# Optimization experiments

Hardware: AMD Instinct MI355X
Metric: run time of the kernel (lower is better)

## Reference

```python
import jax, jax.numpy as jnp
import numpy as np

EPS = 1e-5


def _conv1x1(h, w, b):
    # 1x1 conv == per-pixel matmul: (b,c,h,w) x (o,c) -> (b,o,h,w)
    return jnp.einsum('bchw,oc->bohw', h, w) + b[None, :, None, None]


def setup_inputs() -> dict:
    key = jax.random.key(0)
    ks = jax.random.split(key, 7)
    B, C, H, W = 4, 512, 64, 64
    s = 0.02
    return {
        'x': jax.random.normal(ks[0], (B, C, H, W), dtype=jnp.float32),
        'wq': jax.random.normal(ks[1], (C, C), dtype=jnp.float32) * s,
        'bq': jax.random.normal(ks[2], (C,), dtype=jnp.float32) * s,
        'wk': jax.random.normal(ks[3], (C, C), dtype=jnp.float32) * s,
        'bk': jax.random.normal(ks[4], (C,), dtype=jnp.float32) * s,
        'wv': jax.random.normal(ks[5], (C, C), dtype=jnp.float32) * s,
        'bv': jax.random.normal(ks[6], (C,), dtype=jnp.float32) * s,
    }


def reference(x, wq, bq, wk, bk, wv, bv):
    B, C, H, W = x.shape
    # InstanceNorm2d (affine=False): normalize over spatial dims per (b, c)
    mu = jnp.mean(x, axis=(2, 3), keepdims=True)
    var = jnp.var(x, axis=(2, 3), keepdims=True)  # biased, matches torch
    h_ = (x - mu) * jax.lax.rsqrt(var + EPS)

    q = _conv1x1(h_, wq, bq).reshape(B, C, H * W)  # (b, c, n)
    k = _conv1x1(h_, wk, bk).reshape(B, C, H * W)
    v = _conv1x1(h_, wv, bv).reshape(B, C, H * W)

    scale = float(int(C)) ** (-0.5)
    attn = jnp.einsum('bcq,bck->bqk', q, k) * scale  # (b, n_q, n_k)
    attn = jax.nn.softmax(attn, axis=-1)
    # torch: bmm(v, attn.permute(0,2,1)) -> A[b,c,q] = sum_k v[b,c,k] * attn[b,q,k]
    A = jnp.einsum('bck,bqk->bcq', v, attn).reshape(B, C, H, W)
    return x + A
```

## Files before the change

### kernel.cpp

```cpp
#include <hip/hip_runtime.h>
#include <hip/hip_bf16.h>
#include <cstdint>

#define B_ 4
#define C_ 512
#define N_ 4096

typedef unsigned short u16;
typedef __bf16 bf16x8 __attribute__((ext_vector_type(8)));
typedef float f32x4 __attribute__((ext_vector_type(4)));

union U16B { uint4 u; bf16x8 v; };

__device__ __forceinline__ bf16x8 ld16g(const u16* p) {
  U16B t; t.u = *(const uint4*)p; return t.v;
}

__device__ __forceinline__ u16 f2bf(float f) {
  uint32_t u = __builtin_bit_cast(uint32_t, f);
  u = (u + 0x7FFFu + ((u >> 16) & 1u)) >> 16;
  return (u16)u;
}
__device__ __forceinline__ float bf2f(u16 h) {
  uint32_t u = ((uint32_t)h) << 16;
  return __builtin_bit_cast(float, u);
}

typedef const __attribute__((address_space(1))) uint32_t* gas_p;
typedef __attribute__((address_space(3))) uint32_t* las_p;
__device__ __forceinline__ void gld16(const void* g, void* l) {
  __builtin_amdgcn_global_load_lds((gas_p)g, (las_p)l, 16, 0, 0);
}

#define SCEXP 0.06376149809794171f

__global__ __launch_bounds__(256) void cvt_w(const float* __restrict__ w, u16* __restrict__ o) {
  int i = blockIdx.x * 256 + threadIdx.x;
  float4 v = ((const float4*)w)[i];
  ushort4 r;
  r.x = f2bf(v.x); r.y = f2bf(v.y); r.z = f2bf(v.z); r.w = f2bf(v.w);
  ((ushort4*)o)[i] = r;
}

__global__ __launch_bounds__(1024) void pack_bias(const float* __restrict__ bq,
    const float* __restrict__ bk, float* __restrict__ o) {
  int i = threadIdx.x;
  o[i] = (i < 512) ? bq[i] : bk[i - 512];
}

__global__ __launch_bounds__(256) void inorm_stats(const float* __restrict__ x,
    float* __restrict__ mu, float* __restrict__ rstd) {
  int bc = blockIdx.x;
  const float4* p = (const float4*)(x + (size_t)bc * N_);
  float s = 0.f, ss = 0.f;
  for (int i = threadIdx.x; i < N_ / 4; i += 256) {
    float4 v = p[i];
    s  += v.x + v.y + v.z + v.w;
    ss += v.x * v.x + v.y * v.y + v.z * v.z + v.w * v.w;
  }
#pragma unroll
  for (int off = 32; off > 0; off >>= 1) {
    s  += __shfl_down(s, off);
    ss += __shfl_down(ss, off);
  }
  __shared__ float as_[4], ass_[4];
  if ((threadIdx.x & 63) == 0) { as_[threadIdx.x >> 6] = s; ass_[threadIdx.x >> 6] = ss; }
  __syncthreads();
  if (threadIdx.x == 0) {
    float S  = as_[0] + as_[1] + as_[2] + as_[3];
    float SS = ass_[0] + ass_[1] + ass_[2] + ass_[3];
    float m  = S * (1.f / N_);
    float var = SS * (1.f / N_) - m * m;
    mu[bc] = m;
    rstd[bc] = rsqrtf(var + 1e-5f);
  }
}

__global__ __launch_bounds__(256) void norm_transpose(const float* __restrict__ x,
    const float* __restrict__ mu, const float* __restrict__ rstd, u16* __restrict__ hT) {
  __shared__ u16 tile[64][66];
  int b = blockIdx.z, c0 = blockIdx.y * 64, n0 = blockIdx.x * 64;
  int tn = threadIdx.x & 63, t4 = threadIdx.x >> 6;
  const float* xb = x + ((size_t)b * C_ + c0) * N_ + n0;
#pragma unroll
  for (int it = 0; it < 16; ++it) {
    int c = t4 + it * 4;
    float m  = mu[b * C_ + c0 + c];
    float rs = rstd[b * C_ + c0 + c];
    tile[c][tn] = f2bf((xb[(size_t)c * N_ + tn] - m) * rs);
  }
  __syncthreads();
  u16* hTb = hT + ((size_t)b * N_ + n0) * C_ + c0;
#pragma unroll
  for (int it = 0; it < 16; ++it) {
    int n = t4 + it * 4;
    hTb[(size_t)n * C_ + tn] = tile[tn][n];
  }
}

#define EPI_BCOL 0
#define EPI_BROW 1

template<int EPI>
__global__ __launch_bounds__(256) void gemm128(
    const u16* __restrict__ A, const u16* __restrict__ B,
    const float* __restrict__ aux, void* __restrict__ Out,
    int klen, int lda, int ldb, int ldo,
    long sAz, long sBz, long sOz)
{
  int z = blockIdx.z;
  const u16* Ab = A + (size_t)z * sAz;
  const u16* Bb = B + (size_t)z * sBz;
  int m0 = blockIdx.x * 128, n0 = blockIdx.y * 128;
  int t = threadIdx.x, w = t >> 6, l = t & 63;
  int wr = w >> 1, wc = w & 1;
  int l16 = l & 15, lg = l >> 4;

  __shared__ char smem[65536];

  int srow = t >> 3;
  int scol = ((t & 7) << 4) ^ ((srow & 7) << 4);
  size_t ldaB = (size_t)lda * 2, ldbB = (size_t)ldb * 2;

  f32x4 acc[4][4] = {};
  int nsteps = klen >> 6;

#define STAGE(step, d) {                                                     \
    size_t kbyte = (size_t)(step) * 128 + scol;                              \
    char* lb = smem + (d) * 32768;                                           \
    _Pragma("unroll")                                                        \
    for (int i = 0; i < 4; ++i) {                                            \
      int row = i * 32 + srow;                                               \
      gld16((const char*)Ab + (size_t)(m0 + row) * ldaB + kbyte,             \
            lb + (size_t)(i * 256 + t) * 16);                                \
      gld16((const char*)Bb + (size_t)(n0 + row) * ldbB + kbyte,             \
            lb + 16384 + (size_t)(i * 256 + t) * 16);                        \
    }                                                                        \
  }

  STAGE(0, 0);
  __syncthreads();
  int cur = 0;
  int sw = (l16 & 7) << 4;
  for (int s = 0; s < nsteps; ++s) {
    if (s + 1 < nsteps) STAGE(s + 1, cur ^ 1);
    const char* Al = smem + cur * 32768;
    const char* Bl = Al + 16384;
#pragma unroll
    for (int kc = 0; kc < 2; ++kc) {
      int cb = (kc * 64 + lg * 16) ^ sw;
      bf16x8 af[4], bf[4];
#pragma unroll
      for (int mf = 0; mf < 4; ++mf)
        af[mf] = *(const bf16x8*)(Al + (wr * 64 + mf * 16 + l16) * 128 + cb);
#pragma unroll
      for (int nf = 0; nf < 4; ++nf)
        bf[nf] = *(const bf16x8*)(Bl + (wc * 64 + nf * 16 + l16) * 128 + cb);
#pragma unroll
      for (int mf = 0; mf < 4; ++mf)
#pragma unroll
        for (int nf = 0; nf < 4; ++nf)
          acc[mf][nf] = __builtin_amdgcn_mfma_f32_16x16x32_bf16(af[mf], bf[nf], acc[mf][nf], 0, 0, 0);
    }
    __syncthreads();
    cur ^= 1;
  }
#undef STAGE

  u16* ob = (u16*)Out + (size_t)z * sOz;
  float bc[4];
  if constexpr (EPI == EPI_BCOL) {
#pragma unroll
    for (int nf = 0; nf < 4; ++nf) bc[nf] = aux[n0 + wc * 64 + nf * 16 + l16];
  }
#pragma unroll
  for (int mf = 0; mf < 4; ++mf) {
#pragma unroll
    for (int nf = 0; nf < 4; ++nf) {
      int col = n0 + wc * 64 + nf * 16 + l16;
#pragma unroll
      for (int r = 0; r < 4; ++r) {
        int row = m0 + wr * 64 + mf * 16 + lg * 4 + r;
        float v = acc[mf][nf][r] + (EPI == EPI_BCOL ? bc[nf] : aux[row]);
        ob[(size_t)row * ldo + col] = f2bf(v);
      }
    }
  }
}


#define STG32(Ab, Bb, ldab, step, lb) {                                      \
    size_t kb = (size_t)(step) * 64;                                         \
    _Pragma("unroll")                                                        \
    for (int i = 0; i < 2; ++i) {                                            \
      int s2 = i * 256 + t;                                                  \
      int row = s2 >> 2;                                                     \
      int sc = (((s2 & 3) ^ ((row >> 1) & 3)) & 3) << 4;                     \
      gld16((const char*)(Ab) + (size_t)(m0 + row) * (ldab) + kb + sc,       \
            (lb) + (size_t)s2 * 16);                                         \
      gld16((const char*)(Bb) + (size_t)(n0 + row) * (ldab) + kb + sc,       \
            (lb) + 8192 + (size_t)s2 * 16);                                  \
    }                                                                        \
  }

#define COMP32(lb) {                                                         \
    const char* Al = (lb);                                                   \
    const char* Bl = (lb) + 8192;                                            \
    bf16x8 af[4], bf[4];                                                     \
    _Pragma("unroll")                                                        \
    for (int mf = 0; mf < 4; ++mf)                                           \
      af[mf] = *(const bf16x8*)(Al + (wr * 64 + mf * 16 + l16) * 64 + rg);   \
    _Pragma("unroll")                                                        \
    for (int nf = 0; nf < 4; ++nf)                                           \
      bf[nf] = *(const bf16x8*)(Bl + (wc * 64 + nf * 16 + l16) * 64 + rg);   \
    _Pragma("unroll")                                                        \
    for (int mf = 0; mf < 4; ++mf)                                           \
      _Pragma("unroll")                                                      \
      for (int nf = 0; nf < 4; ++nf)                                         \
        acc[mf][nf] = __builtin_amdgcn_mfma_f32_16x16x32_bf16(af[mf], bf[nf], acc[mf][nf], 0, 0, 0); \
  }

__global__ __launch_bounds__(256, 3) void exp128(
    const u16* __restrict__ qk, float* __restrict__ dsumAll, u16* __restrict__ Pall)
{
  int fid = blockIdx.x;
  int rid = (fid & 7) * 512 + (fid >> 3);
  int z = rid >> 10;
  int r10 = rid & 1023;
  int st = r10 >> 6, w6 = r10 & 63;
  int m0 = ((st >> 2) * 8 + (w6 >> 3)) * 128;
  int n0 = ((st & 3) * 8 + (w6 & 7)) * 128;

  const u16* Ab = qk + (size_t)z * ((size_t)N_ * 1024);
  const u16* Bb = Ab + 512;
  float* dsum = dsumAll + (size_t)z * N_;
  u16* Pp = Pall + (size_t)z * (size_t)N_ * N_;

  int t = threadIdx.x, w = t >> 6, l = t & 63;
  int wr = w >> 1, wc = w & 1;
  int l16 = l & 15, lg = l >> 4;

  __shared__ char smem[49152];

  f32x4 acc[4][4] = {};
  int rg = ((lg ^ ((l16 >> 1) & 3)) & 3) << 4;

  char* buf0 = smem;
  char* buf1 = smem + 16384;
  char* buf2 = smem + 32768;

  STG32(Ab, Bb, 2048, 0, buf0);
  STG32(Ab, Bb, 2048, 1, buf1);
#pragma unroll
  for (int s = 0; s < 15; ++s) {
    asm volatile("s_waitcnt vmcnt(4)" ::: "memory");
    __builtin_amdgcn_s_barrier();
    __builtin_amdgcn_sched_barrier(0);
    if (s + 2 < 16) STG32(Ab, Bb, 2048, s + 2, buf2);
    COMP32(buf0);
    char* tmp = buf0; buf0 = buf1; buf1 = buf2; buf2 = tmp;
  }
  asm volatile("s_waitcnt vmcnt(0)" ::: "memory");
  __builtin_amdgcn_s_barrier();
  __builtin_amdgcn_sched_barrier(0);
  COMP32(buf0);

  __syncthreads();
#pragma unroll
  for (int mf = 0; mf < 4; ++mf) {
#pragma unroll
    for (int r = 0; r < 4; ++r) {
      int row = wr * 64 + mf * 16 + lg * 4 + r;
      int swz = ((row >> 2) & 3) << 5;
      float rs = 0.f;
#pragma unroll
      for (int nf = 0; nf < 4; ++nf) {
        int colb = wc * 128 + nf * 32 + l16 * 2;
        float p = __builtin_amdgcn_exp2f(acc[mf][nf][r] * SCEXP);
        u16 pb = f2bf(p);
        *(u16*)(smem + row * 256 + (colb ^ swz)) = pb;
        rs += bf2f(pb);
      }
      rs += __shfl_xor(rs, 1); rs += __shfl_xor(rs, 2);
      rs += __shfl_xor(rs, 4); rs += __shfl_xor(rs, 8);
      if (l16 == 0) atomicAdd(&dsum[m0 + row], rs);
    }
  }
  __syncthreads();
#pragma unroll
  for (int it = 0; it < 8; ++it) {
    int idx = it * 256 + t;
    int row = idx >> 4, g = idx & 15;
    uint4 v = *(const uint4*)(smem + row * 256 + ((g * 16) ^ (((row >> 2) & 3) << 5)));
    *(uint4*)(Pp + ((size_t)(m0 + row) * N_ + n0 + g * 8)) = v;
  }
}

__global__ __launch_bounds__(256, 3) void pv128(
    const u16* __restrict__ vM, const u16* __restrict__ P,
    const float* __restrict__ denom, const float* __restrict__ x,
    float* __restrict__ out)
{
  int fid = blockIdx.x;
  int rid = (fid & 7) * 64 + (fid >> 3);
  int z = rid >> 7;
  int r7 = rid & 127;
  int n0 = (r7 >> 2) * 128;
  int m0 = (r7 & 3) * 128;

  const u16* Ab = vM + (size_t)z * ((size_t)C_ * N_);
  const u16* Bb = P + (size_t)z * ((size_t)N_ * N_);
  const float* db = denom + (size_t)z * N_;
  const float* xb = x + (size_t)z * ((size_t)C_ * N_);
  float* ob = out + (size_t)z * ((size_t)C_ * N_);

  int t = threadIdx.x, w = t >> 6, l = t & 63;
  int wr = w >> 1, wc = w & 1;
  int l16 = l & 15, lg = l >> 4;

  __shared__ char smem[49152];

  f32x4 acc[4][4] = {};
  int rg = ((lg ^ ((l16 >> 1) & 3)) & 3) << 4;

  char* buf0 = smem;
  char* buf1 = smem + 16384;
  char* buf2 = smem + 32768;

  STG32(Ab, Bb, 8192, 0, buf0);
  STG32(Ab, Bb, 8192, 1, buf1);
#pragma unroll 3
  for (int s = 0; s < 127; ++s) {
    asm volatile("s_waitcnt vmcnt(4)" ::: "memory");
    __builtin_amdgcn_s_barrier();
    __builtin_amdgcn_sched_barrier(0);
    if (s + 2 < 128) STG32(Ab, Bb, 8192, s + 2, buf2);
    COMP32(buf0);
    char* tmp = buf0; buf0 = buf1; buf1 = buf2; buf2 = tmp;
  }
  asm volatile("s_waitcnt vmcnt(0)" ::: "memory");
  __builtin_amdgcn_s_barrier();
  __builtin_amdgcn_sched_barrier(0);
  COMP32(buf0);

  float rd[4];
#pragma unroll
  for (int nf = 0; nf < 4; ++nf)
    rd[nf] = 1.0f / db[n0 + wc * 64 + nf * 16 + l16];
#pragma unroll
  for (int mf = 0; mf < 4; ++mf) {
#pragma unroll
    for (int r = 0; r < 4; ++r) {
      int row = m0 + wr * 64 + mf * 16 + lg * 4 + r;
#pragma unroll
      for (int nf = 0; nf < 4; ++nf) {
        int col = n0 + wc * 64 + nf * 16 + l16;
        size_t o = (size_t)row * N_ + col;
        ob[o] = xb[o] + acc[mf][nf][r] * rd[nf];
      }
    }
  }
}

__global__ __launch_bounds__(256) void gemm_abT(
    const u16* __restrict__ A, const u16* __restrict__ Bm,
    const float* __restrict__ bias, u16* __restrict__ out,
    int ldo, int bias_is_row)
{
  int w = threadIdx.x >> 6, l = threadIdx.x & 63;
  int l16 = l & 15, lg = l >> 4;
  int m0 = blockIdx.x * 128 + (w >> 1) * 64;
  int n0 = blockIdx.y * 128 + (w & 1) * 64;
  f32x4 acc[4][4] = {};
  const u16* Ab = A  + (size_t)(m0 + l16) * 512 + lg * 8;
  const u16* Bb = Bm + (size_t)(n0 + l16) * 512 + lg * 8;
  for (int kc = 0; kc < 512; kc += 32) {
    bf16x8 af[4], bf[4];
#pragma unroll
    for (int i = 0; i < 4; ++i) af[i] = ld16g(Ab + (size_t)(i * 16) * 512 + kc);
#pragma unroll
    for (int j = 0; j < 4; ++j) bf[j] = ld16g(Bb + (size_t)(j * 16) * 512 + kc);
#pragma unroll
    for (int i = 0; i < 4; ++i)
#pragma unroll
      for (int j = 0; j < 4; ++j)
        acc[i][j] = __builtin_amdgcn_mfma_f32_16x16x32_bf16(af[i], bf[j], acc[i][j], 0, 0, 0);
  }
#pragma unroll
  for (int i = 0; i < 4; ++i) {
#pragma unroll
    for (int j = 0; j < 4; ++j) {
      int col = n0 + j * 16 + l16;
#pragma unroll
      for (int r = 0; r < 4; ++r) {
        int row = m0 + i * 16 + lg * 4 + r;
        float v = acc[i][j][r] + (bias_is_row ? bias[row] : bias[col]);
        out[(size_t)row * ldo + col] = f2bf(v);
      }
    }
  }
}

#define NQ 32
#define NKB 64
__global__ __launch_bounds__(512) void attn_kernel(
    const u16* __restrict__ qT, const u16* __restrict__ kT, const u16* __restrict__ vM,
    const float* __restrict__ x, float* __restrict__ out)
{
  int b = blockIdx.y;
  int nq0 = blockIdx.x * NQ;
  const u16* qTb = qT + (size_t)b * N_ * C_;
  const u16* kTb = kT + (size_t)b * N_ * C_;
  const u16* vb  = vM + (size_t)b * C_ * N_;
  const float* xb = x + (size_t)b * C_ * N_;
  float* ob = out + (size_t)b * C_ * N_;

  int tid = threadIdx.x;
  int w = tid >> 6, l = tid & 63, l16 = l & 15, lg = l >> 4;
  int nqf = w & 1, nkf = w >> 1;
  int c0 = w * 64;

  __shared__ u16 qlds[32][520];
  __shared__ u16 Plds[32][72];
  __shared__ float dpart[32][16];
  __shared__ float dfin[32];

  for (int idx = tid; idx < 32 * 64; idx += 512) {
    int row = idx >> 6, cg = idx & 63;
    *(uint4*)&qlds[row][cg * 8] = *(const uint4*)(qTb + (size_t)(nq0 + row) * C_ + cg * 8);
  }
  __syncthreads();

  f32x4 acc[2][4] = {};
  float dreg = 0.f;
  int drow = tid >> 4, dcol = (tid & 15) * 4;

  for (int nk0 = 0; nk0 < N_; nk0 += NKB) {
    f32x4 s = {0.f, 0.f, 0.f, 0.f};
    const u16* krow = kTb + (size_t)(nk0 + nkf * 16 + l16) * C_ + lg * 8;
#pragma unroll 4
    for (int kc = 0; kc < 16; ++kc) {
      U16B tq; tq.u = *(const uint4*)&qlds[nqf * 16 + l16][kc * 32 + lg * 8];
      bf16x8 kf = ld16g(krow + kc * 32);
      s = __builtin_amdgcn_mfma_f32_16x16x32_bf16(tq.v, kf, s, 0, 0, 0);
    }
    __syncthreads();
#pragma unroll
    for (int r = 0; r < 4; ++r) {
      float p = __builtin_amdgcn_exp2f(s[r] * SCEXP);
      Plds[nqf * 16 + lg * 4 + r][nkf * 16 + l16] = f2bf(p);
    }
    __syncthreads();
#pragma unroll
    for (int r = 0; r < 4; ++r) dreg += bf2f(Plds[drow][dcol + r]);
#pragma unroll
    for (int kk = 0; kk < 2; ++kk) {
      bf16x8 pf[2];
#pragma unroll
      for (int i = 0; i < 2; ++i) {
        U16B t2; t2.u = *(const uint4*)&Plds[i * 16 + l16][kk * 32 + lg * 8];
        pf[i] = t2.v;
      }
#pragma unroll
      for (int j = 0; j < 4; ++j) {
        bf16x8 vf = ld16g(vb + (size_t)(c0 + j * 16 + l16) * N_ + nk0 + kk * 32 + lg * 8);
#pragma unroll
        for (int i = 0; i < 2; ++i)
          acc[i][j] = __builtin_amdgcn_mfma_f32_16x16x32_bf16(pf[i], vf, acc[i][j], 0, 0, 0);
      }
    }
  }

  dpart[drow][tid & 15] = dreg;
  __syncthreads();
  if (tid < 32) {
    float s2 = 0.f;
#pragma unroll
    for (int g = 0; g < 16; ++g) s2 += dpart[tid][g];
    dfin[tid] = s2;
  }
  __syncthreads();

#pragma unroll
  for (int i = 0; i < 2; ++i) {
    float dinv[4];
#pragma unroll
    for (int r = 0; r < 4; ++r) dinv[r] = 1.f / dfin[i * 16 + lg * 4 + r];
    int nbase = nq0 + i * 16 + lg * 4;
#pragma unroll
    for (int j = 0; j < 4; ++j) {
      int c = c0 + j * 16 + l16;
      float4 xv = *(const float4*)(xb + (size_t)c * N_ + nbase);
      float4 o;
      o.x = xv.x + acc[i][j][0] * dinv[0];
      o.y = xv.y + acc[i][j][1] * dinv[1];
      o.z = xv.z + acc[i][j][2] * dinv[2];
      o.w = xv.w + acc[i][j][3] * dinv[3];
      *(float4*)(ob + (size_t)c * N_ + nbase) = o;
    }
  }
}

extern "C" void kernel_launch(void* const* d_in, const int* in_sizes, int n_in,
                              void* d_out, int out_size, void* d_ws, size_t ws_size,
                              hipStream_t stream) {
  (void)in_sizes; (void)n_in; (void)out_size;
  const float* x  = (const float*)d_in[0];
  const float* wq = (const float*)d_in[1];
  const float* bq = (const float*)d_in[2];
  const float* wk = (const float*)d_in[3];
  const float* bk = (const float*)d_in[4];
  const float* wv = (const float*)d_in[5];
  const float* bv = (const float*)d_in[6];
  float* out = (float*)d_out;
  char* ws = (char*)d_ws;

  const size_t NC = (size_t)N_ * C_;
  const size_t NEED = 203489280;

  if (ws_size >= NEED) {
    u16*   wbf_q = (u16*)(ws);
    u16*   wbf_k = (u16*)(ws + 524288);
    u16*   wbf_v = (u16*)(ws + 1048576);
    float* bqk   = (float*)(ws + 1572864);
    float* mu    = (float*)(ws + 1581056);
    float* rstd  = (float*)(ws + 1589248);
    u16*   hT    = (u16*)(ws + 1597440);
    u16*   qkT   = (u16*)(ws + 18874368);
    u16*   vM    = (u16*)(ws + 52428800);
    float* denom = (float*)(ws + 69206016);
    u16*   P     = (u16*)(ws + 69271552);

    cvt_w<<<256, 256, 0, stream>>>(wq, wbf_q);
    cvt_w<<<256, 256, 0, stream>>>(wk, wbf_k);
    cvt_w<<<256, 256, 0, stream>>>(wv, wbf_v);
    pack_bias<<<1, 1024, 0, stream>>>(bq, bk, bqk);
    inorm_stats<<<B_ * C_, 256, 0, stream>>>(x, mu, rstd);
    norm_transpose<<<dim3(N_ / 64, C_ / 64, B_), 256, 0, stream>>>(x, mu, rstd, hT);
    hipMemsetAsync(denom, 0, 4 * N_ * sizeof(float), stream);

    gemm128<EPI_BCOL><<<dim3(32, 8, 4), 256, 0, stream>>>(
        hT, wbf_q, bqk, qkT, 512, 512, 512, 1024, (long)NC, 0, (long)N_ * 1024);
    gemm128<EPI_BROW><<<dim3(4, 32, 4), 256, 0, stream>>>(
        wbf_v, hT, bv, vM, 512, 512, 512, 4096, 0, (long)NC, (long)NC);

    exp128<<<4096, 256, 0, stream>>>(qkT, denom, P);

    pv128<<<512, 256, 0, stream>>>(vM, P, denom, x, out);
  } else {
    u16*   wbf_q = (u16*)(ws);
    u16*   wbf_k = (u16*)(ws + 524288);
    u16*   wbf_v = (u16*)(ws + 1048576);
    float* mu    = (float*)(ws + 1572864);
    float* rstd  = (float*)(ws + 1581056);
    u16*   hT    = (u16*)(ws + 1589248);
    u16*   qT    = (u16*)(ws + 18366464);
    u16*   kT    = (u16*)(ws + 35143680);
    u16*   vM    = (u16*)(ws + 51920896);

    cvt_w<<<256, 256, 0, stream>>>(wq, wbf_q);
    cvt_w<<<256, 256, 0, stream>>>(wk, wbf_k);
    cvt_w<<<256, 256, 0, stream>>>(wv, wbf_v);
    inorm_stats<<<B_ * C_, 256, 0, stream>>>(x, mu, rstd);
    norm_transpose<<<dim3(N_ / 64, C_ / 64, B_), 256, 0, stream>>>(x, mu, rstd, hT);

    for (int b = 0; b < B_; ++b) {
      const u16* hTb = hT + (size_t)b * NC;
      u16* qTb = qT + (size_t)b * NC;
      u16* kTb = kT + (size_t)b * NC;
      u16* vMb = vM + (size_t)b * NC;
      gemm_abT<<<dim3(N_ / 128, C_ / 128), 256, 0, stream>>>(hTb, wbf_q, bq, qTb, C_, 0);
      gemm_abT<<<dim3(N_ / 128, C_ / 128), 256, 0, stream>>>(hTb, wbf_k, bk, kTb, C_, 0);
      gemm_abT<<<dim3(C_ / 128, N_ / 128), 256, 0, stream>>>(wbf_v, hTb, bv, vMb, N_, 1);
    }
    attn_kernel<<<dim3(N_ / NQ, B_), 512, 0, stream>>>(qT, kT, vM, x, out);
  }
}
```

Measured before the change: 240.8 us.

## Widen QK^T exp kernel tile to 128x256 with four column-split waves

Replaces the 128x128 score/exp kernel with a 128x256 tile where each of four waves owns a 64-column strip and all 128 rows, doubling per-wave accumulators. This halves the number of blocks and the re-reading of the Q tile per output, improving arithmetic intensity of the K-loop. It costs more registers and LDS (72KB), lowers occupancy to 2 blocks/SM, and changes the block swizzle mapping.

```diff
diff --git a/kernel.cpp b/kernel.cpp
--- a/kernel.cpp
+++ b/kernel.cpp
@@ -220,16 +220,16 @@
         acc[mf][nf] = __builtin_amdgcn_mfma_f32_16x16x32_bf16(af[mf], bf[nf], acc[mf][nf], 0, 0, 0); \
   }
 
-__global__ __launch_bounds__(256, 3) void exp128(
+__global__ __launch_bounds__(256, 2) void exp_wide(
     const u16* __restrict__ qk, float* __restrict__ dsumAll, u16* __restrict__ Pall)
 {
   int fid = blockIdx.x;
-  int rid = (fid & 7) * 512 + (fid >> 3);
-  int z = rid >> 10;
-  int r10 = rid & 1023;
-  int st = r10 >> 6, w6 = r10 & 63;
-  int m0 = ((st >> 2) * 8 + (w6 >> 3)) * 128;
-  int n0 = ((st & 3) * 8 + (w6 & 7)) * 128;
+  int rid = (fid & 7) * 256 + (fid >> 3);
+  int z = rid >> 9;
+  int r9 = rid & 511;
+  int st = r9 >> 6, w6 = r9 & 63;
+  int m0 = ((st >> 1) * 8 + (w6 >> 3)) * 128;
+  int n0 = ((st & 1) * 8 + (w6 & 7)) * 256;
 
   const u16* Ab = qk + (size_t)z * ((size_t)N_ * 1024);
   const u16* Bb = Ab + 512;
@@ -237,40 +237,79 @@
   u16* Pp = Pall + (size_t)z * (size_t)N_ * N_;
 
   int t = threadIdx.x, w = t >> 6, l = t & 63;
-  int wr = w >> 1, wc = w & 1;
+  int wc = w;
   int l16 = l & 15, lg = l >> 4;
 
-  __shared__ char smem[49152];
-
-  f32x4 acc[4][4] = {};
+  __shared__ char smem[73728];
+
+  f32x4 acc[8][4] = {};
   int rg = ((lg ^ ((l16 >> 1) & 3)) & 3) << 4;
 
+#define STGW(step, lb) {                                                     \
+    size_t kb = (size_t)(step) * 64;                                         \
+    _Pragma("unroll")                                                        \
+    for (int i = 0; i < 2; ++i) {                                            \
+      int s2 = i * 256 + t;                                                  \
+      int row = s2 >> 2;                                                     \
+      int sc = (((s2 & 3) ^ ((row >> 1) & 3)) & 3) << 4;                     \
+      gld16((const char*)Ab + (size_t)(m0 + row) * 2048 + kb + sc,           \
+            (lb) + (size_t)s2 * 16);                                         \
+    }                                                                        \
+    _Pragma("unroll")                                                        \
+    for (int i = 0; i < 4; ++i) {                                            \
+      int s2 = i * 256 + t;                                                  \
+      int row = s2 >> 2;                                                     \
+      int sc = (((s2 & 3) ^ ((row >> 1) & 3)) & 3) << 4;                     \
+      gld16((const char*)Bb + (size_t)(n0 + row) * 2048 + kb + sc,           \
+            (lb) + 8192 + (size_t)s2 * 16);                                  \
+    }                                                                        \
+  }
+
+#define COMPW(lb) {                                                         \
+    const char* Al = (lb);                                                  \
+    const char* Bl = (lb) + 8192;                                           \
+    bf16x8 af[8], bf[4];                                                    \
+    _Pragma("unroll")                                                       \
+    for (int mf = 0; mf < 8; ++mf)                                          \
+      af[mf] = *(const bf16x8*)(Al + (mf * 16 + l16) * 64 + rg);            \
+    _Pragma("unroll")                                                       \
+    for (int nf = 0; nf < 4; ++nf)                                          \
+      bf[nf] = *(const bf16x8*)(Bl + (wc * 64 + nf * 16 + l16) * 64 + rg);  \
+    _Pragma("unroll")                                                       \
+    for (int mf = 0; mf < 8; ++mf)                                          \
+      _Pragma("unroll")                                                     \
+      for (int nf = 0; nf < 4; ++nf)                                        \
+        acc[mf][nf] = __builtin_amdgcn_mfma_f32_16x16x32_bf16(af[mf], bf[nf], acc[mf][nf], 0, 0, 0); \
+  }
+
   char* buf0 = smem;
-  char* buf1 = smem + 16384;
-  char* buf2 = smem + 32768;
-
-  STG32(Ab, Bb, 2048, 0, buf0);
-  STG32(Ab, Bb, 2048, 1, buf1);
-#pragma unroll
+  char* buf1 = smem + 24576;
+  char* buf2 = smem + 49152;
+
+  STGW(0, buf0);
+  STGW(1, buf1);
+#pragma unroll 3
   for (int s = 0; s < 15; ++s) {
-    asm volatile("s_waitcnt vmcnt(4)" ::: "memory");
+    asm volatile("s_waitcnt vmcnt(6)" ::: "memory");
     __builtin_amdgcn_s_barrier();
     __builtin_amdgcn_sched_barrier(0);
-    if (s + 2 < 16) STG32(Ab, Bb, 2048, s + 2, buf2);
-    COMP32(buf0);
+    if (s + 2 < 16) STGW(s + 2, buf2);
+    COMPW(buf0);
     char* tmp = buf0; buf0 = buf1; buf1 = buf2; buf2 = tmp;
   }
   asm volatile("s_waitcnt vmcnt(0)" ::: "memory");
   __builtin_amdgcn_s_barrier();
   __builtin_amdgcn_sched_barrier(0);
-  COMP32(buf0);
-
-  __syncthreads();
-#pragma unroll
-  for (int mf = 0; mf < 4; ++mf) {
+  COMPW(buf0);
+#undef STGW
+#undef COMPW
+
+  __syncthreads();
+#pragma unroll
+  for (int mf = 0; mf < 8; ++mf) {
 #pragma unroll
     for (int r = 0; r < 4; ++r) {
-      int row = wr * 64 + mf * 16 + lg * 4 + r;
+      int row = mf * 16 + lg * 4 + r;
       int swz = ((row >> 2) & 3) << 5;
       float rs = 0.f;
 #pragma unroll
@@ -278,7 +317,7 @@
         int colb = wc * 128 + nf * 32 + l16 * 2;
         float p = __builtin_amdgcn_exp2f(acc[mf][nf][r] * SCEXP);
         u16 pb = f2bf(p);
-        *(u16*)(smem + row * 256 + (colb ^ swz)) = pb;
+        *(u16*)(smem + row * 512 + (colb ^ swz)) = pb;
         rs += bf2f(pb);
       }
       rs += __shfl_xor(rs, 1); rs += __shfl_xor(rs, 2);
@@ -288,10 +327,10 @@
   }
   __syncthreads();
 #pragma unroll
-  for (int it = 0; it < 8; ++it) {
+  for (int it = 0; it < 16; ++it) {
     int idx = it * 256 + t;
-    int row = idx >> 4, g = idx & 15;
-    uint4 v = *(const uint4*)(smem + row * 256 + ((g * 16) ^ (((row >> 2) & 3) << 5)));
+    int row = idx >> 5, g = idx & 31;
+    uint4 v = *(const uint4*)(smem + row * 512 + ((g * 16) ^ (((row >> 2) & 3) << 5)));
     *(uint4*)(Pp + ((size_t)(m0 + row) * N_ + n0 + g * 8)) = v;
   }
 }
@@ -544,7 +583,7 @@
     gemm128<EPI_BROW><<<dim3(4, 32, 4), 256, 0, stream>>>(
         wbf_v, hT, bv, vM, 512, 512, 512, 4096, 0, (long)NC, (long)NC);
 
-    exp128<<<4096, 256, 0, stream>>>(qkT, denom, P);
+    exp_wide<<<2048, 256, 0, stream>>>(qkT, denom, P);
 
     pv128<<<512, 256, 0, stream>>>(vM, P, denom, x, out);
   } else {
```

Result: slower. 254.5 us (+5.7%).

## Store Q/K in FP8 and compute attention scores with FP8 MFMA

Applied to the files above, without the earlier changes.

The Q/K projection epilogue now writes FP8 (e4m3) values with a byte-permuted layout through shared memory, halving the size of the QK buffer. The score kernel is rewritten as exp8, which uses fp8 MFMA instructions, 512-thread blocks with 128x256 tiles and double buffering instead of triple buffering. This cuts global traffic and MFMA time for the QK^T stage, at the cost of reduced precision in the attention logits, which may hurt accuracy.

```diff
diff --git a/kernel.cpp b/kernel.cpp
--- a/kernel.cpp
+++ b/kernel.cpp
@@ -7,6 +7,7 @@
 #define N_ 4096
 
 typedef unsigned short u16;
+typedef unsigned char u8;
 typedef __bf16 bf16x8 __attribute__((ext_vector_type(8)));
 typedef float f32x4 __attribute__((ext_vector_type(4)));
 
@@ -24,6 +25,20 @@
 __device__ __forceinline__ float bf2f(u16 h) {
   uint32_t u = ((uint32_t)h) << 16;
   return __builtin_bit_cast(float, u);
+}
+
+__device__ __forceinline__ u8 f2fp8(float f) {
+  uint32_t u = __builtin_bit_cast(uint32_t, f);
+  uint32_t s = (u >> 24) & 0x80u;
+  uint32_t a = u & 0x7FFFFFFFu;
+  if (a >= 0x43700000u) return (u8)(s | 0x7E);
+  if (a < 0x3C800000u) {
+    float af = __builtin_bit_cast(float, a);
+    int m = (int)(af * 512.0f + 0.5f);
+    return (u8)(s | (uint32_t)m);
+  }
+  uint32_t r = (a + 0x7FFFFu + ((a >> 20) & 1u)) >> 20;
+  return (u8)(s | (r - (120u << 3)));
 }
 
 typedef const __attribute__((address_space(1))) uint32_t* gas_p;
@@ -98,8 +113,8 @@
   }
 }
 
-#define EPI_BCOL 0
 #define EPI_BROW 1
+#define EPI_QK8  2
 
 template<int EPI>
 __global__ __launch_bounds__(256) void gemm128(
@@ -167,27 +182,51 @@
   }
 #undef STAGE
 
-  u16* ob = (u16*)Out + (size_t)z * sOz;
-  float bc[4];
-  if constexpr (EPI == EPI_BCOL) {
+  if constexpr (EPI == EPI_BROW) {
+    u16* ob = (u16*)Out + (size_t)z * sOz;
+#pragma unroll
+    for (int mf = 0; mf < 4; ++mf) {
+#pragma unroll
+      for (int nf = 0; nf < 4; ++nf) {
+        int col = n0 + wc * 64 + nf * 16 + l16;
+#pragma unroll
+        for (int r = 0; r < 4; ++r) {
+          int row = m0 + wr * 64 + mf * 16 + lg * 4 + r;
+          float v = acc[mf][nf][r] + aux[row];
+          ob[(size_t)row * ldo + col] = f2bf(v);
+        }
+      }
+    }
+  } else {
+    u8* ob = (u8*)Out + (size_t)z * sOz;
+    char* sb = smem;
+    float bc[4];
 #pragma unroll
     for (int nf = 0; nf < 4; ++nf) bc[nf] = aux[n0 + wc * 64 + nf * 16 + l16];
-  }
-#pragma unroll
-  for (int mf = 0; mf < 4; ++mf) {
-#pragma unroll
-    for (int nf = 0; nf < 4; ++nf) {
-      int col = n0 + wc * 64 + nf * 16 + l16;
-#pragma unroll
-      for (int r = 0; r < 4; ++r) {
-        int row = m0 + wr * 64 + mf * 16 + lg * 4 + r;
-        float v = acc[mf][nf][r] + (EPI == EPI_BCOL ? bc[nf] : aux[row]);
-        ob[(size_t)row * ldo + col] = f2bf(v);
+#pragma unroll
+    for (int mf = 0; mf < 4; ++mf) {
+#pragma unroll
+      for (int nf = 0; nf < 4; ++nf) {
+        int cl = wc * 64 + nf * 16 + l16;
+        int w6 = cl & 63;
+        int clp = (cl & 64) | (((w6 >> 3) & 3) * 16) | (((w6 >> 5) & 1) * 8) | (w6 & 7);
+#pragma unroll
+        for (int r = 0; r < 4; ++r) {
+          int rowl = wr * 64 + mf * 16 + lg * 4 + r;
+          sb[rowl * 128 + clp] = (char)f2fp8(acc[mf][nf][r] + bc[nf]);
+        }
       }
     }
-  }
-}
-
+    __syncthreads();
+#pragma unroll
+    for (int it = 0; it < 4; ++it) {
+      int idx = it * 256 + t;
+      int row = idx >> 3, seg = idx & 7;
+      *(uint4*)(ob + (size_t)(m0 + row) * ldo + n0 + seg * 16) =
+          *(const uint4*)(sb + row * 128 + seg * 16);
+    }
+  }
+}
 
 #define STG32(Ab, Bb, ldab, step, lb) {                                      \
     size_t kb = (size_t)(step) * 64;                                         \
@@ -220,52 +259,101 @@
         acc[mf][nf] = __builtin_amdgcn_mfma_f32_16x16x32_bf16(af[mf], bf[nf], acc[mf][nf], 0, 0, 0); \
   }
 
-__global__ __launch_bounds__(256, 3) void exp128(
-    const u16* __restrict__ qk, float* __restrict__ dsumAll, u16* __restrict__ Pall)
+__global__ __launch_bounds__(512, 2) void exp8(
+    const u8* __restrict__ qk8, float* __restrict__ dsumAll, u16* __restrict__ Pall)
 {
   int fid = blockIdx.x;
-  int rid = (fid & 7) * 512 + (fid >> 3);
-  int z = rid >> 10;
-  int r10 = rid & 1023;
-  int st = r10 >> 6, w6 = r10 & 63;
-  int m0 = ((st >> 2) * 8 + (w6 >> 3)) * 128;
-  int n0 = ((st & 3) * 8 + (w6 & 7)) * 128;
-
-  const u16* Ab = qk + (size_t)z * ((size_t)N_ * 1024);
-  const u16* Bb = Ab + 512;
+  int rid = (fid & 7) * 256 + (fid >> 3);
+  int z = rid >> 9;
+  int r9 = rid & 511;
+  int c2 = r9 >> 8;
+  int r8 = r9 & 255;
+  int sm = r8 >> 6, w6s = r8 & 63;
+  int m0 = (c2 * 16 + (sm >> 1) * 8 + (w6s >> 3)) * 128;
+  int n0 = ((sm & 1) * 8 + (w6s & 7)) * 256;
+
+  const u8* Ab = qk8 + (size_t)z * ((size_t)N_ * 1024);
+  const u8* Bb = Ab + 512;
   float* dsum = dsumAll + (size_t)z * N_;
   u16* Pp = Pall + (size_t)z * (size_t)N_ * N_;
 
   int t = threadIdx.x, w = t >> 6, l = t & 63;
-  int wr = w >> 1, wc = w & 1;
+  int wr = w >> 2, wc = w & 3;
   int l16 = l & 15, lg = l >> 4;
 
-  __shared__ char smem[49152];
+  __shared__ char smem[65536];
 
   f32x4 acc[4][4] = {};
   int rg = ((lg ^ ((l16 >> 1) & 3)) & 3) << 4;
 
+#define STG8(step, lb) {                                                     \
+    size_t kb = (size_t)(step) * 64;                                         \
+    {                                                                        \
+      int row = t >> 2, g = t & 3;                                           \
+      int sg = (g ^ ((row >> 1) & 3)) << 4;                                  \
+      gld16((const char*)Ab + (size_t)(m0 + row) * 1024 + kb + sg,           \
+            (lb) + (size_t)t * 16);                                          \
+    }                                                                        \
+    _Pragma("unroll")                                                        \
+    for (int i = 0; i < 2; ++i) {                                            \
+      int s2 = i * 512 + t;                                                  \
+      int row = s2 >> 2, g = s2 & 3;                                         \
+      int sg = (g ^ ((row >> 1) & 3)) << 4;                                  \
+      gld16((const char*)Bb + (size_t)(n0 + row) * 1024 + kb + sg,           \
+            (lb) + 8192 + (size_t)s2 * 16);                                  \
+    }                                                                        \
+  }
+
+#define COMP8(lb) {                                                          \
+    const char* Al = (lb);                                                   \
+    const char* Bl = (lb) + 8192;                                            \
+    uint4 af[4], bf[4];                                                      \
+    _Pragma("unroll")                                                        \
+    for (int mf = 0; mf < 4; ++mf)                                           \
+      af[mf] = *(const uint4*)(Al + (wr * 64 + mf * 16 + l16) * 64 + rg);    \
+    _Pragma("unroll")                                                        \
+    for (int nf = 0; nf < 4; ++nf)                                           \
+      bf[nf] = *(const uint4*)(Bl + (wc * 64 + nf * 16 + l16) * 64 + rg);    \
+    _Pragma("unroll")                                                        \
+    for (int kk = 0; kk < 2; ++kk) {                                         \
+      _Pragma("unroll")                                                      \
+      for (int mf = 0; mf < 4; ++mf) {                                       \
+        long long a8 = ((long long)(kk ? af[mf].w : af[mf].y) << 32) |       \
+                       (unsigned int)(kk ? af[mf].z : af[mf].x);             \
+        _Pragma("unroll")                                                    \
+        for (int nf = 0; nf < 4; ++nf) {                                     \
+          long long b8 = ((long long)(kk ? bf[nf].w : bf[nf].y) << 32) |     \
+                         (unsigned int)(kk ? bf[nf].z : bf[nf].x);           \
+          acc[mf][nf] = __builtin_amdgcn_mfma_f32_16x16x32_fp8_fp8(          \
+              a8, b8, acc[mf][nf], 0, 0, 0);                                 \
+        }                                                                    \
+      }                                                                      \
+    }                                                                        \
+  }
+
   char* buf0 = smem;
-  char* buf1 = smem + 16384;
-  char* buf2 = smem + 32768;
-
-  STG32(Ab, Bb, 2048, 0, buf0);
-  STG32(Ab, Bb, 2048, 1, buf1);
-#pragma unroll
-  for (int s = 0; s < 15; ++s) {
-    asm volatile("s_waitcnt vmcnt(4)" ::: "memory");
+  char* buf1 = smem + 24576;
+
+  STG8(0, buf0);
+#pragma unroll
+  for (int s = 0; s < 8; ++s) {
+    char* cb = (s & 1) ? buf1 : buf0;
+    char* nb = (s & 1) ? buf0 : buf1;
+    if (s < 7) {
+      STG8(s + 1, nb);
+      asm volatile("s_waitcnt vmcnt(3)" ::: "memory");
+    } else {
+      asm volatile("s_waitcnt vmcnt(0)" ::: "memory");
+    }
     __builtin_amdgcn_s_barrier();
     __builtin_amdgcn_sched_barrier(0);
-    if (s + 2 < 16) STG32(Ab, Bb, 2048, s + 2, buf2);
-    COMP32(buf0);
-    char* tmp = buf0; buf0 = buf1; buf1 = buf2; buf2 = tmp;
-  }
-  asm volatile("s_waitcnt vmcnt(0)" ::: "memory");
-  __builtin_amdgcn_s_barrier();
-  __builtin_amdgcn_sched_barrier(0);
-  COMP32(buf0);
-
-  __syncthreads();
+    COMP8(cb);
+    __builtin_amdgcn_sched_barrier(0);
+    __builtin_amdgcn_s_barrier();
+  }
+#undef STG8
+#undef COMP8
+
 #pragma unroll
   for (int mf = 0; mf < 4; ++mf) {
 #pragma unroll
@@ -278,7 +366,7 @@
         int colb = wc * 128 + nf * 32 + l16 * 2;
         float p = __builtin_amdgcn_exp2f(acc[mf][nf][r] * SCEXP);
         u16 pb = f2bf(p);
-        *(u16*)(smem + row * 256 + (colb ^ swz)) = pb;
+        *(u16*)(smem + row * 512 + (colb ^ swz)) = pb;
         rs += bf2f(pb);
       }
       rs += __shfl_xor(rs, 1); rs += __shfl_xor(rs, 2);
@@ -289,9 +377,9 @@
   __syncthreads();
 #pragma unroll
   for (int it = 0; it < 8; ++it) {
-    int idx = it * 256 + t;
-    int row = idx >> 4, g = idx & 15;
-    uint4 v = *(const uint4*)(smem + row * 256 + ((g * 16) ^ (((row >> 2) & 3) << 5)));
+    int idx = it * 512 + t;
+    int row = idx >> 5, g = idx & 31;
+    uint4 v = *(const uint4*)(smem + row * 512 + ((g * 16) ^ (((row >> 2) & 3) << 5)));
     *(uint4*)(Pp + ((size_t)(m0 + row) * N_ + n0 + g * 8)) = v;
   }
 }
@@ -526,7 +614,7 @@
     float* mu    = (float*)(ws + 1581056);
     float* rstd  = (float*)(ws + 1589248);
     u16*   hT    = (u16*)(ws + 1597440);
-    u16*   qkT   = (u16*)(ws + 18874368);
+    u8*    qk8   = (u8*)(ws + 18874368);
     u16*   vM    = (u16*)(ws + 52428800);
     float* denom = (float*)(ws + 69206016);
     u16*   P     = (u16*)(ws + 69271552);
@@ -539,12 +627,12 @@
     norm_transpose<<<dim3(N_ / 64, C_ / 64, B_), 256, 0, stream>>>(x, mu, rstd, hT);
     hipMemsetAsync(denom, 0, 4 * N_ * sizeof(float), stream);
 
-    gemm128<EPI_BCOL><<<dim3(32, 8, 4), 256, 0, stream>>>(
-        hT, wbf_q, bqk, qkT, 512, 512, 512, 1024, (long)NC, 0, (long)N_ * 1024);
+    gemm128<EPI_QK8><<<dim3(32, 8, 4), 256, 0, stream>>>(
+        hT, wbf_q, bqk, qk8, 512, 512, 512, 1024, (long)NC, 0, (long)N_ * 1024);
     gemm128<EPI_BROW><<<dim3(4, 32, 4), 256, 0, stream>>>(
         wbf_v, hT, bv, vM, 512, 512, 512, 4096, 0, (long)NC, (long)NC);
 
-    exp128<<<4096, 256, 0, stream>>>(qkT, denom, P);
+    exp8<<<2048, 512, 0, stream>>>(qk8, denom, P);
 
     pv128<<<512, 256, 0, stream>>>(vM, P, denom, x, out);
   } else {
```

Result: faster. 233.9 us (-2.9%).
